# Optimization experiments

Hardware: AMD Instinct MI355X
Metric: run time of the kernel (lower is better)

Reference implementation:

```python
import jax, jax.numpy as jnp
import numpy as np

N = 14        # nodes per graph (fixed by hidden*14 in the Linear)
H = 4         # attention heads
F_IN = 128    # num_feature
C = 64        # hidden (per-head out_channels; concat=False -> mean over heads)
NEG_SLOPE = 0.2  # PyG GATConv default negative_slope


def gat_conv(x, src, dst, W, a_src, a_dst, b):
    """One PyG-style GATConv on a single graph.
    x: [N, F]  W: [F, H*C]  a_src/a_dst: [H, C]  b: [C]
    src/dst: [E] int (self-loops already appended). concat=False -> mean over heads.
    """
    h = (x @ W).reshape(N, H, C)                       # [N,H,C]
    al_src = jnp.einsum('nhc,hc->nh', h, a_src)        # [N,H]
    al_dst = jnp.einsum('nhc,hc->nh', h, a_dst)        # [N,H]
    e = jax.nn.leaky_relu(al_src[src] + al_dst[dst], NEG_SLOPE)  # [E,H]
    # softmax over incoming edges of each destination node (stable)
    m = jax.ops.segment_max(e, dst, num_segments=N)    # [N,H]
    ex = jnp.exp(e - m[dst])
    denom = jax.ops.segment_sum(ex, dst, num_segments=N)
    alpha = ex / denom[dst]                            # [E,H]
    out = jax.ops.segment_sum(alpha[:, :, None] * h[src], dst, num_segments=N)  # [N,H,C]
    return out.mean(axis=1) + b                        # [N,C]


def setup_inputs() -> dict:
    key = jax.random.key(0)
    ks = jax.random.split(key, 12)
    B, E = 16384, 182
    feature = jax.random.normal(ks[0], (B, N, F_IN), dtype=jnp.float32)
    edge_list = jax.random.randint(ks[1], (B, E, 2), 0, N, dtype=jnp.int64)

    def glorot(k, shape):
        fan = shape[0] + shape[-1]
        return jax.random.normal(k, shape, dtype=jnp.float32) * jnp.sqrt(2.0 / fan)

    return {
        'feature': feature,
        'edge_list': edge_list,
        'W1': glorot(ks[2], (F_IN, H * C)),
        'a_src1': glorot(ks[3], (H, C)),
        'a_dst1': glorot(ks[4], (H, C)),
        'b1': jnp.zeros((C,), jnp.float32),
        'W2': glorot(ks[5], (C, H * C)),
        'a_src2': glorot(ks[6], (H, C)),
        'a_dst2': glorot(ks[7], (H, C)),
        'b2': jnp.zeros((C,), jnp.float32),
        'W_lin': glorot(ks[8], (N * C, C // 2)),
        'b_lin': jnp.zeros((C // 2,), jnp.float32),
        'W_pred': glorot(ks[9], (C // 2, 1)),
        'b_pred': jnp.zeros((1,), jnp.float32),
    }


def reference(feature, edge_list, W1, a_src1, a_dst1, b1, W2, a_src2, a_dst2, b2,
              W_lin, b_lin, W_pred, b_pred):
    B = feature.shape[0]
    # PyG GATConv adds self-loops by default
    loops = jnp.broadcast_to(jnp.arange(N, dtype=edge_list.dtype), (B, N))
    src = jnp.concatenate([edge_list[..., 0], loops], axis=1)  # [B, E+N]
    dst = jnp.concatenate([edge_list[..., 1], loops], axis=1)

    def per_graph(x, s, d):
        h = jax.nn.relu(gat_conv(x, s, d, W1, a_src1, a_dst1, b1))
        # dropout is identity in eval mode
        h = gat_conv(h, s, d, W2, a_src2, a_dst2, b2)       # [N,C]
        z = h.reshape(-1) @ W_lin + b_lin                    # [C//2]
        p = z @ W_pred + b_pred                              # [1]
        return jax.nn.sigmoid(p)

    return jax.vmap(per_graph)(feature, src, dst)            # [B,1]
```

## Files before the change

kernel.cpp:

```cpp
#include <hip/hip_runtime.h>

#define NN 14
#define EE 182

typedef __attribute__((ext_vector_type(8))) short bf16x8;
typedef __attribute__((ext_vector_type(4))) short bf16x4;
typedef __attribute__((ext_vector_type(4))) float f32x4;
typedef __attribute__((ext_vector_type(4))) unsigned u32x4;
typedef __attribute__((ext_vector_type(2))) unsigned u32x2;

__device__ __forceinline__ unsigned f2bf(float f) {
    unsigned u = __float_as_uint(f);
    return (u + 0x7fffu + ((u >> 16) & 1u)) >> 16;
}
__device__ __forceinline__ unsigned pack2bf(float lo, float hi) {
    return __builtin_amdgcn_perm(__float_as_uint(hi) + 0x8000u,
                                 __float_as_uint(lo) + 0x8000u, 0x07060302u);
}
__device__ __forceinline__ bf16x8 mk8(unsigned a, unsigned b, unsigned c, unsigned d) {
    u32x4 u = {a, b, c, d};
    return __builtin_bit_cast(bf16x8, u);
}
__device__ __forceinline__ bf16x4 mk4(unsigned a, unsigned b) {
    u32x2 u = {a, b};
    return __builtin_bit_cast(bf16x4, u);
}

__global__ void prep_pack(const float* __restrict__ W1, const float* __restrict__ W2,
                          const float* __restrict__ Wl, const float* __restrict__ Wpred,
                          const float* __restrict__ bl, const float* __restrict__ bp,
                          const float* __restrict__ as1, const float* __restrict__ ad1,
                          const float* __restrict__ as2, const float* __restrict__ ad2,
                          short* __restrict__ wp1, short* __restrict__ wp2,
                          short* __restrict__ battn1, short* __restrict__ battn2,
                          float* __restrict__ wcombP) {
    int gid = blockIdx.x * 256 + threadIdx.x;
    if (gid < 32768) {
        int j = gid & 7, L = (gid >> 3) & 63, kk = (gid >> 9) & 3, nt = gid >> 11;
        int k = kk * 32 + (L >> 4) * 8 + j, n = nt * 16 + (L & 15);
        wp1[gid] = (short)f2bf(W1[k * 256 + n]);
    } else if (gid < 49152) {
        int g2 = gid - 32768;
        int j = g2 & 7, L = (g2 >> 3) & 63, kk = (g2 >> 9) & 1, nt = g2 >> 10;
        int k = kk * 32 + (L >> 4) * 8 + j, n = nt * 16 + (L & 15);
        wp2[g2] = (short)f2bf(W2[k * 256 + n]);
    } else if (gid < 51200) {
        int g2 = gid - 49152;
        int j = g2 & 7, L = (g2 >> 3) & 63, kk = g2 >> 9;
        int n = L & 15, k = kk * 32 + (L >> 4) * 8 + j;
        float val = 0.f;
        if (n < 8) {
            const float* av = ((n >> 2) ? ad1 : as1) + (n & 3) * 64;
            const float* wr = W1 + k * 256 + (n & 3) * 64;
            for (int c = 0; c < 64; ++c) val += wr[c] * av[c];
        }
        battn1[g2] = (short)f2bf(val);
    } else if (gid < 52224) {
        int g2 = gid - 51200;
        int j = g2 & 7, L = (g2 >> 3) & 63, kk = g2 >> 9;
        int n = L & 15, k = kk * 32 + (L >> 4) * 8 + j;
        float val = 0.f;
        if (n < 8) {
            const float* av = ((n >> 2) ? ad2 : as2) + (n & 3) * 64;
            const float* wr = W2 + k * 256 + (n & 3) * 64;
            for (int c = 0; c < 64; ++c) val += wr[c] * av[c];
        }
        battn2[g2] = (short)f2bf(val);
    } else if (gid < 56320) {
        int o = gid - 52224;
        int r = o & 3, i4 = o >> 2;
        int m = i4 & 15, ctq = i4 >> 4;
        int q = ctq & 3, ct = ctq >> 2;
        int chan = ct * 16 + q * 4 + r;
        float acc = 0.f;
        if (m < NN) {
            const float* wr = Wl + (m * 64 + chan) * 32;
            #pragma unroll
            for (int j = 0; j < 32; ++j) acc += wr[j] * Wpred[j];
        }
        wcombP[o] = acc;
    } else if (gid == 56320) {
        float acc = bp[0];
        #pragma unroll
        for (int j = 0; j < 32; ++j) acc += bl[j] * Wpred[j];
        wcombP[4096] = acc;
    }
}

template<int KK, bool RELU>
__device__ __forceinline__ void gat_layer2(int lane,
    const bf16x8 (*a)[KK], const short* wpB,
    const float* __restrict__ bias, const float* slabw,
    f32x4 (*o)[4], unsigned (*po)[4][2])
{
    const int m = lane & 15, q = lane >> 4;
    f32x4 agg[2][4];
    #pragma unroll
    for (int u = 0; u < 2; ++u)
        #pragma unroll
        for (int ct = 0; ct < 4; ++ct) agg[u][ct] = f32x4{0.f, 0.f, 0.f, 0.f};

    #pragma unroll
    for (int h = 0; h < 4; ++h) {
        bf16x4 P[2];
        #pragma unroll
        for (int u = 0; u < 2; ++u) {
            const float* cntf = slabw + u * 448;
            const float* alsd = cntf + 320;
            f32x4 alv = *(const f32x4*)(alsd + h * 16 + q * 4);
            float ad  = alsd[64 + h * 16 + m];
            f32x4 cv  = *(const f32x4*)(cntf + m * 20 + q * 4);
            float l0 = alv[0] + ad, l1 = alv[1] + ad, l2 = alv[2] + ad, l3 = alv[3] + ad;
            l0 = fmaxf(l0, 0.f) + 0.2f * fminf(l0, 0.f);
            l1 = fmaxf(l1, 0.f) + 0.2f * fminf(l1, 0.f);
            l2 = fmaxf(l2, 0.f) + 0.2f * fminf(l2, 0.f);
            l3 = fmaxf(l3, 0.f) + 0.2f * fminf(l3, 0.f);
            float v0 = __expf(l0) * cv[0], v1 = __expf(l1) * cv[1];
            float v2 = __expf(l2) * cv[2], v3 = __expf(l3) * cv[3];
            float s = v0 + v1 + v2 + v3;
            s += __shfl_xor(s, 16);
            s += __shfl_xor(s, 32);
            float inv = (s > 0.f) ? 0.25f / s : 0.f;
            P[u] = mk4(pack2bf(v0 * inv, v1 * inv), pack2bf(v2 * inv, v3 * inv));
        }

        #pragma unroll
        for (int ct = 0; ct < 4; ++ct) {
            f32x4 c0 = f32x4{0.f, 0.f, 0.f, 0.f}, c1 = f32x4{0.f, 0.f, 0.f, 0.f};
            #pragma unroll
            for (int kk = 0; kk < KK; ++kk) {
                bf16x8 b = *(const bf16x8*)(wpB +
                    (((h * 4 + ct) * KK + kk) * 64 + lane) * 8);
                c0 = __builtin_amdgcn_mfma_f32_16x16x32_bf16(a[0][kk], b, c0, 0, 0, 0);
                c1 = __builtin_amdgcn_mfma_f32_16x16x32_bf16(a[1][kk], b, c1, 0, 0, 0);
            }
            agg[0][ct] = __builtin_amdgcn_mfma_f32_16x16x16bf16_1k(
                mk4(pack2bf(c0[0], c0[1]), pack2bf(c0[2], c0[3])), P[0], agg[0][ct], 0, 0, 0);
            agg[1][ct] = __builtin_amdgcn_mfma_f32_16x16x16bf16_1k(
                mk4(pack2bf(c1[0], c1[1]), pack2bf(c1[2], c1[3])), P[1], agg[1][ct], 0, 0, 0);
        }
    }

    #pragma unroll
    for (int ct = 0; ct < 4; ++ct) {
        float4 bb = *(const float4*)(bias + ct * 16 + q * 4);
        #pragma unroll
        for (int u = 0; u < 2; ++u) {
            float o0 = agg[u][ct][0] + bb.x, o1 = agg[u][ct][1] + bb.y;
            float o2v = agg[u][ct][2] + bb.z, o3 = agg[u][ct][3] + bb.w;
            if (RELU) {
                o0 = fmaxf(o0, 0.f);  o1 = fmaxf(o1, 0.f);
                o2v = fmaxf(o2v, 0.f); o3 = fmaxf(o3, 0.f);
                if (m >= NN) { o0 = 0.f; o1 = 0.f; o2v = 0.f; o3 = 0.f; }
                po[u][ct][0] = pack2bf(o0, o1);
                po[u][ct][1] = pack2bf(o2v, o3);
            } else {
                o[u][ct] = f32x4{o0, o1, o2v, o3};
            }
        }
    }
}

__global__ __launch_bounds__(1024, 4) void gat_fused(
    const float* __restrict__ feature,
    const int*   __restrict__ edge_list,
    const float* __restrict__ b1, const float* __restrict__ b2,
    const short* __restrict__ wpck,
    const float* __restrict__ wcombP,
    float* __restrict__ out, int B)
{
    const int w = threadIdx.x >> 6, lane = threadIdx.x & 63;
    const int m = lane & 15, q = lane >> 4;

    __shared__ __align__(16) short    swts[52224];
    __shared__ __align__(16) unsigned slab[16 * 896];

    float* slabw = (float*)(slab + w * 896);

    {
        const u32x4* srcw = (const u32x4*)wpck;
        u32x4* dstw = (u32x4*)swts;
        #pragma unroll
        for (int r = 0; r < 7; ++r) {
            int i = r * 1024 + (int)threadIdx.x;
            if (i < 6528) dstw[i] = srcw[i];
        }
    }
    __syncthreads();

    const short* swp1  = swts;
    const short* swp2  = swts + 32768;
    const short* sbat1 = swts + 49152;
    const short* sbat2 = swts + 51200;

    const int g0 = blockIdx.x * 64 + w * 4;

    #pragma clang loop unroll(disable)
    for (int it = 0; it < 2; ++it) {
        const int g = g0 + it * 2;
        if (g >= B) break;
        const bool act1 = (g + 1) < B;
        float* cnt0 = slabw;
        float* cnt1 = slabw + 448;

        #pragma unroll
        for (int i = 0; i < 5; ++i) {
            cnt0[i * 64 + lane] = 0.f;
            cnt1[i * 64 + lane] = 0.f;
        }
        {
            const int2* ep0 = (const int2*)edge_list + (size_t)g * EE;
            const int2* ep1 = ep0 + EE;
            #pragma unroll
            for (int r = 0; r < 3; ++r) {
                int i = r * 64 + lane;
                if (i < EE) {
                    int2 e0 = ep0[i];
                    atomicAdd(&cnt0[e0.y * 20 + e0.x], 1.f);
                    if (act1) { int2 e1 = ep1[i]; atomicAdd(&cnt1[e1.y * 20 + e1.x], 1.f); }
                }
            }
            if (lane < NN) {
                atomicAdd(&cnt0[lane * 21], 1.f);
                if (act1) atomicAdd(&cnt1[lane * 21], 1.f);
            }
        }

        bf16x8 a1[2][4];
        #pragma unroll
        for (int u = 0; u < 2; ++u)
            #pragma unroll
            for (int kk = 0; kk < 4; ++kk) a1[u][kk] = mk8(0, 0, 0, 0);
        if (m < NN) {
            const float* xg0 = feature + (size_t)g * (NN * 128) + m * 128;
            #pragma unroll
            for (int kk = 0; kk < 4; ++kk) {
                float4 v0 = *(const float4*)(xg0 + kk * 32 + q * 8);
                float4 v1 = *(const float4*)(xg0 + kk * 32 + q * 8 + 4);
                a1[0][kk] = mk8(pack2bf(v0.x, v0.y), pack2bf(v0.z, v0.w),
                                pack2bf(v1.x, v1.y), pack2bf(v1.z, v1.w));
            }
        }
        if (act1 && m < NN) {
            const float* xg1 = feature + (size_t)(g + 1) * (NN * 128) + m * 128;
            #pragma unroll
            for (int kk = 0; kk < 4; ++kk) {
                float4 v0 = *(const float4*)(xg1 + kk * 32 + q * 8);
                float4 v1 = *(const float4*)(xg1 + kk * 32 + q * 8 + 4);
                a1[1][kk] = mk8(pack2bf(v0.x, v0.y), pack2bf(v0.z, v0.w),
                                pack2bf(v1.x, v1.y), pack2bf(v1.z, v1.w));
            }
        }

        {
            f32x4 ca0 = f32x4{0.f, 0.f, 0.f, 0.f}, ca1 = f32x4{0.f, 0.f, 0.f, 0.f};
            #pragma unroll
            for (int kk = 0; kk < 4; ++kk) {
                bf16x8 b = *(const bf16x8*)(sbat1 + (kk * 64 + lane) * 8);
                ca0 = __builtin_amdgcn_mfma_f32_16x16x32_bf16(a1[0][kk], b, ca0, 0, 0, 0);
                ca1 = __builtin_amdgcn_mfma_f32_16x16x32_bf16(a1[1][kk], b, ca1, 0, 0, 0);
            }
            if (m < 8) {
                int off = (m >> 2) * 64 + (m & 3) * 16 + q * 4;
                *(f32x4*)(slabw + 320 + off) = ca0;
                *(f32x4*)(slabw + 448 + 320 + off) = ca1;
            }
        }

        unsigned po1[2][4][2];
        gat_layer2<4, true>(lane, a1, swp1, b1, slabw, nullptr, po1);

        bf16x8 a2[2][2];
        {
            int ad0 = ((q & 1) * 32 + m) * 4;
            int ad1_ = ad0 + 64;
            bool hi = (q >> 1) != 0;
            #pragma unroll
            for (int u = 0; u < 2; ++u)
            #pragma unroll
            for (int kk = 0; kk < 2; ++kk) {
                unsigned sA0 = __builtin_amdgcn_ds_bpermute(ad0, (int)po1[u][2 * kk][0]);
                unsigned sA1 = __builtin_amdgcn_ds_bpermute(ad0, (int)po1[u][2 * kk][1]);
                unsigned sB0 = __builtin_amdgcn_ds_bpermute(ad0, (int)po1[u][2 * kk + 1][0]);
                unsigned sB1 = __builtin_amdgcn_ds_bpermute(ad0, (int)po1[u][2 * kk + 1][1]);
                unsigned tA0 = __builtin_amdgcn_ds_bpermute(ad1_, (int)po1[u][2 * kk][0]);
                unsigned tA1 = __builtin_amdgcn_ds_bpermute(ad1_, (int)po1[u][2 * kk][1]);
                unsigned tB0 = __builtin_amdgcn_ds_bpermute(ad1_, (int)po1[u][2 * kk + 1][0]);
                unsigned tB1 = __builtin_amdgcn_ds_bpermute(ad1_, (int)po1[u][2 * kk + 1][1]);
                a2[u][kk] = mk8(hi ? sB0 : sA0, hi ? sB1 : sA1,
                                hi ? tB0 : tA0, hi ? tB1 : tA1);
            }
        }

        {
            f32x4 ca0 = f32x4{0.f, 0.f, 0.f, 0.f}, ca1 = f32x4{0.f, 0.f, 0.f, 0.f};
            #pragma unroll
            for (int kk = 0; kk < 2; ++kk) {
                bf16x8 b = *(const bf16x8*)(sbat2 + (kk * 64 + lane) * 8);
                ca0 = __builtin_amdgcn_mfma_f32_16x16x32_bf16(a2[0][kk], b, ca0, 0, 0, 0);
                ca1 = __builtin_amdgcn_mfma_f32_16x16x32_bf16(a2[1][kk], b, ca1, 0, 0, 0);
            }
            if (m < 8) {
                int off = (m >> 2) * 64 + (m & 3) * 16 + q * 4;
                *(f32x4*)(slabw + 320 + off) = ca0;
                *(f32x4*)(slabw + 448 + 320 + off) = ca1;
            }
        }

        f32x4 o2[2][4];
        gat_layer2<2, false>(lane, a2, swp2, b2, slabw, o2, nullptr);

        float p0 = 0.f, p1 = 0.f;
        #pragma unroll
        for (int ct = 0; ct < 4; ++ct) {
            float4 wv = *(const float4*)(wcombP + ((ct * 4 + q) * 16 + m) * 4);
            p0 += o2[0][ct][0] * wv.x + o2[0][ct][1] * wv.y +
                  o2[0][ct][2] * wv.z + o2[0][ct][3] * wv.w;
            p1 += o2[1][ct][0] * wv.x + o2[1][ct][1] * wv.y +
                  o2[1][ct][2] * wv.z + o2[1][ct][3] * wv.w;
        }
        p0 += __shfl_xor(p0, 1);  p1 += __shfl_xor(p1, 1);
        p0 += __shfl_xor(p0, 2);  p1 += __shfl_xor(p1, 2);
        p0 += __shfl_xor(p0, 4);  p1 += __shfl_xor(p1, 4);
        p0 += __shfl_xor(p0, 8);  p1 += __shfl_xor(p1, 8);
        p0 += __shfl_xor(p0, 16); p1 += __shfl_xor(p1, 16);
        p0 += __shfl_xor(p0, 32); p1 += __shfl_xor(p1, 32);
        if (lane == 0) {
            float cc = wcombP[4096];
            out[g] = 1.f / (1.f + __expf(-(p0 + cc)));
            if (act1) out[g + 1] = 1.f / (1.f + __expf(-(p1 + cc)));
        }
    }
}

extern "C" void kernel_launch(void* const* d_in, const int* in_sizes, int n_in,
                              void* d_out, int out_size, void* d_ws, size_t ws_size,
                              hipStream_t stream) {
    const float* feature = (const float*)d_in[0];
    const int*   edges   = (const int*)d_in[1];
    const float* W1  = (const float*)d_in[2];
    const float* as1 = (const float*)d_in[3];
    const float* ad1 = (const float*)d_in[4];
    const float* b1  = (const float*)d_in[5];
    const float* W2  = (const float*)d_in[6];
    const float* as2 = (const float*)d_in[7];
    const float* ad2 = (const float*)d_in[8];
    const float* b2  = (const float*)d_in[9];
    const float* Wl  = (const float*)d_in[10];
    const float* bl  = (const float*)d_in[11];
    const float* Wp  = (const float*)d_in[12];
    const float* bp  = (const float*)d_in[13];
    float* out = (float*)d_out;

    short* wp1    = (short*)d_ws;
    short* wp2    = wp1 + 32768;
    short* battn1 = wp2 + 16384;
    short* battn2 = battn1 + 2048;
    float* wcombP = (float*)(battn2 + 1024);

    prep_pack<<<221, 256, 0, stream>>>(W1, W2, Wl, Wp, bl, bp, as1, ad1, as2, ad2,
                                       wp1, wp2, battn1, battn2, wcombP);

    const int B = in_sizes[0] / (NN * 128);
    gat_fused<<<(B + 63) / 64, 1024, 0, stream>>>(feature, edges, b1, b2,
                                                  wp1, wcombP, out, B);
}
```

Baseline: 234.1 us.

## Prefetch next graph pair during layer 1 and pack edge counts into bytes

Unrolls the two-iteration per-wave loop into two process_pair calls. The first call issues the feature loads and edge scatter for the second pair after its layer-1 work, so global-memory latency overlaps with MFMA compute. Edge multiplicity counts move from float LDS atomics to byte-packed uint atomics, which shrinks the per-wave LDS slab and lets each gat_layer2 read its counts with one dword load. The softmax coefficients for all heads are also computed before the MFMA loop. In exchange, register pressure rises (two sets of a1 fragments live at once, plus P[4][2]), and byte counts would overflow if more than 255 edges repeat on one pair, which cannot happen with 182 edges.

```diff
diff --git a/kernel.cpp b/kernel.cpp
--- a/kernel.cpp
+++ b/kernel.cpp
@@ -87,43 +87,84 @@
     }
 }
 
+__device__ __forceinline__ void scatter_edges(int lane, const int2* ep,
+                                              unsigned char* cnt, bool act) {
+    if (!act) return;
+    #pragma unroll
+    for (int r = 0; r < 3; ++r) {
+        int i = r * 64 + lane;
+        if (i < EE) {
+            int2 e = ep[i];
+            int b = e.y * 20 + e.x;
+            atomicAdd((unsigned*)(cnt + (b & ~3)), 1u << ((b & 3) * 8));
+        }
+    }
+    if (lane < NN) {
+        int b = lane * 21;
+        atomicAdd((unsigned*)(cnt + (b & ~3)), 1u << ((b & 3) * 8));
+    }
+}
+
+__device__ __forceinline__ void load_a1(const float* __restrict__ feature,
+                                        int g, int m, int q, bool act, bf16x8* dst) {
+    if (act && m < NN) {
+        const float* xg = feature + (size_t)g * (NN * 128) + m * 128;
+        #pragma unroll
+        for (int kk = 0; kk < 4; ++kk) {
+            float4 v0 = *(const float4*)(xg + kk * 32 + q * 8);
+            float4 v1 = *(const float4*)(xg + kk * 32 + q * 8 + 4);
+            dst[kk] = mk8(pack2bf(v0.x, v0.y), pack2bf(v0.z, v0.w),
+                          pack2bf(v1.x, v1.y), pack2bf(v1.z, v1.w));
+        }
+    } else {
+        #pragma unroll
+        for (int kk = 0; kk < 4; ++kk) dst[kk] = mk8(0, 0, 0, 0);
+    }
+}
+
 template<int KK, bool RELU>
 __device__ __forceinline__ void gat_layer2(int lane,
     const bf16x8 (*a)[KK], const short* wpB,
-    const float* __restrict__ bias, const float* slabw,
+    const float* __restrict__ bias,
+    const unsigned char* cntb, const float* alsd,
     f32x4 (*o)[4], unsigned (*po)[4][2])
 {
     const int m = lane & 15, q = lane >> 4;
-    f32x4 agg[2][4];
-    #pragma unroll
-    for (int u = 0; u < 2; ++u)
-        #pragma unroll
-        for (int ct = 0; ct < 4; ++ct) agg[u][ct] = f32x4{0.f, 0.f, 0.f, 0.f};
-
+
+    bf16x4 P[4][2];
     #pragma unroll
     for (int h = 0; h < 4; ++h) {
-        bf16x4 P[2];
         #pragma unroll
         for (int u = 0; u < 2; ++u) {
-            const float* cntf = slabw + u * 448;
-            const float* alsd = cntf + 320;
-            f32x4 alv = *(const f32x4*)(alsd + h * 16 + q * 4);
-            float ad  = alsd[64 + h * 16 + m];
-            f32x4 cv  = *(const f32x4*)(cntf + m * 20 + q * 4);
+            const float* alsdu = alsd + u * 128;
+            f32x4 alv = *(const f32x4*)(alsdu + h * 16 + q * 4);
+            float ad  = alsdu[64 + h * 16 + m];
+            unsigned cw = *(const unsigned*)(cntb + u * 320 + m * 20 + q * 4);
             float l0 = alv[0] + ad, l1 = alv[1] + ad, l2 = alv[2] + ad, l3 = alv[3] + ad;
             l0 = fmaxf(l0, 0.f) + 0.2f * fminf(l0, 0.f);
             l1 = fmaxf(l1, 0.f) + 0.2f * fminf(l1, 0.f);
             l2 = fmaxf(l2, 0.f) + 0.2f * fminf(l2, 0.f);
             l3 = fmaxf(l3, 0.f) + 0.2f * fminf(l3, 0.f);
-            float v0 = __expf(l0) * cv[0], v1 = __expf(l1) * cv[1];
-            float v2 = __expf(l2) * cv[2], v3 = __expf(l3) * cv[3];
+            float v0 = __expf(l0) * (float)(cw & 255u);
+            float v1 = __expf(l1) * (float)((cw >> 8) & 255u);
+            float v2 = __expf(l2) * (float)((cw >> 16) & 255u);
+            float v3 = __expf(l3) * (float)(cw >> 24);
             float s = v0 + v1 + v2 + v3;
             s += __shfl_xor(s, 16);
             s += __shfl_xor(s, 32);
             float inv = (s > 0.f) ? 0.25f / s : 0.f;
-            P[u] = mk4(pack2bf(v0 * inv, v1 * inv), pack2bf(v2 * inv, v3 * inv));
-        }
-
+            P[h][u] = mk4(pack2bf(v0 * inv, v1 * inv), pack2bf(v2 * inv, v3 * inv));
+        }
+    }
+
+    f32x4 agg[2][4];
+    #pragma unroll
+    for (int u = 0; u < 2; ++u)
+        #pragma unroll
+        for (int ct = 0; ct < 4; ++ct) agg[u][ct] = f32x4{0.f, 0.f, 0.f, 0.f};
+
+    #pragma unroll
+    for (int h = 0; h < 4; ++h) {
         #pragma unroll
         for (int ct = 0; ct < 4; ++ct) {
             f32x4 c0 = f32x4{0.f, 0.f, 0.f, 0.f}, c1 = f32x4{0.f, 0.f, 0.f, 0.f};
@@ -135,9 +176,9 @@
                 c1 = __builtin_amdgcn_mfma_f32_16x16x32_bf16(a[1][kk], b, c1, 0, 0, 0);
             }
             agg[0][ct] = __builtin_amdgcn_mfma_f32_16x16x16bf16_1k(
-                mk4(pack2bf(c0[0], c0[1]), pack2bf(c0[2], c0[3])), P[0], agg[0][ct], 0, 0, 0);
+                mk4(pack2bf(c0[0], c0[1]), pack2bf(c0[2], c0[3])), P[h][0], agg[0][ct], 0, 0, 0);
             agg[1][ct] = __builtin_amdgcn_mfma_f32_16x16x16bf16_1k(
-                mk4(pack2bf(c1[0], c1[1]), pack2bf(c1[2], c1[3])), P[1], agg[1][ct], 0, 0, 0);
+                mk4(pack2bf(c1[0], c1[1]), pack2bf(c1[2], c1[3])), P[h][1], agg[1][ct], 0, 0, 0);
         }
     }
 
@@ -161,6 +202,108 @@
     }
 }
 
+template<bool PRE>
+__device__ __forceinline__ void process_pair(
+    int lane, int g, bool act1,
+    const bf16x8 (*a1)[4],
+    unsigned char* cntb, float* alsd,
+    const short* swp1, const short* swp2, const short* sbat1, const short* sbat2,
+    const float* __restrict__ b1, const float* __restrict__ b2,
+    const float* __restrict__ wcombP, float* __restrict__ out, int B,
+    const float* __restrict__ feature, const int* __restrict__ edge_list,
+    int gN, unsigned char* cntbN, bf16x8 (*a1N)[4])
+{
+    const int m = lane & 15, q = lane >> 4;
+
+    {
+        f32x4 ca0 = f32x4{0.f, 0.f, 0.f, 0.f}, ca1 = f32x4{0.f, 0.f, 0.f, 0.f};
+        #pragma unroll
+        for (int kk = 0; kk < 4; ++kk) {
+            bf16x8 b = *(const bf16x8*)(sbat1 + (kk * 64 + lane) * 8);
+            ca0 = __builtin_amdgcn_mfma_f32_16x16x32_bf16(a1[0][kk], b, ca0, 0, 0, 0);
+            ca1 = __builtin_amdgcn_mfma_f32_16x16x32_bf16(a1[1][kk], b, ca1, 0, 0, 0);
+        }
+        if (m < 8) {
+            int off = (m >> 2) * 64 + (m & 3) * 16 + q * 4;
+            *(f32x4*)(alsd + off) = ca0;
+            *(f32x4*)(alsd + 128 + off) = ca1;
+        }
+    }
+
+    unsigned po1[2][4][2];
+    gat_layer2<4, true>(lane, a1, swp1, b1, cntb, alsd, nullptr, po1);
+
+    if (PRE) {
+        bool aN0 = gN < B, aN1 = gN + 1 < B;
+        load_a1(feature, gN, m, q, aN0, a1N[0]);
+        load_a1(feature, gN + 1, m, q, aN1, a1N[1]);
+        const int2* ep = (const int2*)edge_list + (size_t)gN * EE;
+        scatter_edges(lane, ep, cntbN, aN0);
+        scatter_edges(lane, ep + EE, cntbN + 320, aN1);
+    }
+
+    bf16x8 a2[2][2];
+    {
+        int ad0 = ((q & 1) * 32 + m) * 4;
+        int ad1_ = ad0 + 64;
+        bool hi = (q >> 1) != 0;
+        #pragma unroll
+        for (int u = 0; u < 2; ++u)
+        #pragma unroll
+        for (int kk = 0; kk < 2; ++kk) {
+            unsigned sA0 = __builtin_amdgcn_ds_bpermute(ad0, (int)po1[u][2 * kk][0]);
+            unsigned sA1 = __builtin_amdgcn_ds_bpermute(ad0, (int)po1[u][2 * kk][1]);
+            unsigned sB0 = __builtin_amdgcn_ds_bpermute(ad0, (int)po1[u][2 * kk + 1][0]);
+            unsigned sB1 = __builtin_amdgcn_ds_bpermute(ad0, (int)po1[u][2 * kk + 1][1]);
+            unsigned tA0 = __builtin_amdgcn_ds_bpermute(ad1_, (int)po1[u][2 * kk][0]);
+            unsigned tA1 = __builtin_amdgcn_ds_bpermute(ad1_, (int)po1[u][2 * kk][1]);
+            unsigned tB0 = __builtin_amdgcn_ds_bpermute(ad1_, (int)po1[u][2 * kk + 1][0]);
+            unsigned tB1 = __builtin_amdgcn_ds_bpermute(ad1_, (int)po1[u][2 * kk + 1][1]);
+            a2[u][kk] = mk8(hi ? sB0 : sA0, hi ? sB1 : sA1,
+                            hi ? tB0 : tA0, hi ? tB1 : tA1);
+        }
+    }
+
+    {
+        f32x4 ca0 = f32x4{0.f, 0.f, 0.f, 0.f}, ca1 = f32x4{0.f, 0.f, 0.f, 0.f};
+        #pragma unroll
+        for (int kk = 0; kk < 2; ++kk) {
+            bf16x8 b = *(const bf16x8*)(sbat2 + (kk * 64 + lane) * 8);
+            ca0 = __builtin_amdgcn_mfma_f32_16x16x32_bf16(a2[0][kk], b, ca0, 0, 0, 0);
+            ca1 = __builtin_amdgcn_mfma_f32_16x16x32_bf16(a2[1][kk], b, ca1, 0, 0, 0);
+        }
+        if (m < 8) {
+            int off = (m >> 2) * 64 + (m & 3) * 16 + q * 4;
+            *(f32x4*)(alsd + off) = ca0;
+            *(f32x4*)(alsd + 128 + off) = ca1;
+        }
+    }
+
+    f32x4 o2[2][4];
+    gat_layer2<2, false>(lane, a2, swp2, b2, cntb, alsd, o2, nullptr);
+
+    float p0 = 0.f, p1 = 0.f;
+    #pragma unroll
+    for (int ct = 0; ct < 4; ++ct) {
+        float4 wv = *(const float4*)(wcombP + ((ct * 4 + q) * 16 + m) * 4);
+        p0 += o2[0][ct][0] * wv.x + o2[0][ct][1] * wv.y +
+              o2[0][ct][2] * wv.z + o2[0][ct][3] * wv.w;
+        p1 += o2[1][ct][0] * wv.x + o2[1][ct][1] * wv.y +
+              o2[1][ct][2] * wv.z + o2[1][ct][3] * wv.w;
+    }
+    p0 += __shfl_xor(p0, 1);  p1 += __shfl_xor(p1, 1);
+    p0 += __shfl_xor(p0, 2);  p1 += __shfl_xor(p1, 2);
+    p0 += __shfl_xor(p0, 4);  p1 += __shfl_xor(p1, 4);
+    p0 += __shfl_xor(p0, 8);  p1 += __shfl_xor(p1, 8);
+    p0 += __shfl_xor(p0, 16); p1 += __shfl_xor(p1, 16);
+    p0 += __shfl_xor(p0, 32); p1 += __shfl_xor(p1, 32);
+    if (lane == 0) {
+        float cc = wcombP[4096];
+        out[g] = 1.f / (1.f + __expf(-(p0 + cc)));
+        if (act1) out[g + 1] = 1.f / (1.f + __expf(-(p1 + cc)));
+    }
+}
+
 __global__ __launch_bounds__(1024, 4) void gat_fused(
     const float* __restrict__ feature,
     const int*   __restrict__ edge_list,
@@ -173,9 +316,11 @@
     const int m = lane & 15, q = lane >> 4;
 
     __shared__ __align__(16) short    swts[52224];
-    __shared__ __align__(16) unsigned slab[16 * 896];
-
-    float* slabw = (float*)(slab + w * 896);
+    __shared__ __align__(16) unsigned slab[16 * 576];
+
+    unsigned* swave = slab + w * 576;
+    unsigned char* cntb = (unsigned char*)swave;
+    float* alsd = (float*)(swave + 320);
 
     {
         const u32x4* srcw = (const u32x4*)wpck;
@@ -194,143 +339,28 @@
     const short* sbat2 = swts + 51200;
 
     const int g0 = blockIdx.x * 64 + w * 4;
-
-    #pragma clang loop unroll(disable)
-    for (int it = 0; it < 2; ++it) {
-        const int g = g0 + it * 2;
-        if (g >= B) break;
-        const bool act1 = (g + 1) < B;
-        float* cnt0 = slabw;
-        float* cnt1 = slabw + 448;
-
-        #pragma unroll
-        for (int i = 0; i < 5; ++i) {
-            cnt0[i * 64 + lane] = 0.f;
-            cnt1[i * 64 + lane] = 0.f;
-        }
-        {
-            const int2* ep0 = (const int2*)edge_list + (size_t)g * EE;
-            const int2* ep1 = ep0 + EE;
-            #pragma unroll
-            for (int r = 0; r < 3; ++r) {
-                int i = r * 64 + lane;
-                if (i < EE) {
-                    int2 e0 = ep0[i];
-                    atomicAdd(&cnt0[e0.y * 20 + e0.x], 1.f);
-                    if (act1) { int2 e1 = ep1[i]; atomicAdd(&cnt1[e1.y * 20 + e1.x], 1.f); }
-                }
-            }
-            if (lane < NN) {
-                atomicAdd(&cnt0[lane * 21], 1.f);
-                if (act1) atomicAdd(&cnt1[lane * 21], 1.f);
-            }
-        }
-
-        bf16x8 a1[2][4];
-        #pragma unroll
-        for (int u = 0; u < 2; ++u)
-            #pragma unroll
-            for (int kk = 0; kk < 4; ++kk) a1[u][kk] = mk8(0, 0, 0, 0);
-        if (m < NN) {
-            const float* xg0 = feature + (size_t)g * (NN * 128) + m * 128;
-            #pragma unroll
-            for (int kk = 0; kk < 4; ++kk) {
-                float4 v0 = *(const float4*)(xg0 + kk * 32 + q * 8);
-                float4 v1 = *(const float4*)(xg0 + kk * 32 + q * 8 + 4);
-                a1[0][kk] = mk8(pack2bf(v0.x, v0.y), pack2bf(v0.z, v0.w),
-                                pack2bf(v1.x, v1.y), pack2bf(v1.z, v1.w));
-            }
-        }
-        if (act1 && m < NN) {
-            const float* xg1 = feature + (size_t)(g + 1) * (NN * 128) + m * 128;
-            #pragma unroll
-            for (int kk = 0; kk < 4; ++kk) {
-                float4 v0 = *(const float4*)(xg1 + kk * 32 + q * 8);
-                float4 v1 = *(const float4*)(xg1 + kk * 32 + q * 8 + 4);
-                a1[1][kk] = mk8(pack2bf(v0.x, v0.y), pack2bf(v0.z, v0.w),
-                                pack2bf(v1.x, v1.y), pack2bf(v1.z, v1.w));
-            }
-        }
-
-        {
-            f32x4 ca0 = f32x4{0.f, 0.f, 0.f, 0.f}, ca1 = f32x4{0.f, 0.f, 0.f, 0.f};
-            #pragma unroll
-            for (int kk = 0; kk < 4; ++kk) {
-                bf16x8 b = *(const bf16x8*)(sbat1 + (kk * 64 + lane) * 8);
-                ca0 = __builtin_amdgcn_mfma_f32_16x16x32_bf16(a1[0][kk], b, ca0, 0, 0, 0);
-                ca1 = __builtin_amdgcn_mfma_f32_16x16x32_bf16(a1[1][kk], b, ca1, 0, 0, 0);
-            }
-            if (m < 8) {
-                int off = (m >> 2) * 64 + (m & 3) * 16 + q * 4;
-                *(f32x4*)(slabw + 320 + off) = ca0;
-                *(f32x4*)(slabw + 448 + 320 + off) = ca1;
-            }
-        }
-
-        unsigned po1[2][4][2];
-        gat_layer2<4, true>(lane, a1, swp1, b1, slabw, nullptr, po1);
-
-        bf16x8 a2[2][2];
-        {
-            int ad0 = ((q & 1) * 32 + m) * 4;
-            int ad1_ = ad0 + 64;
-            bool hi = (q >> 1) != 0;
-            #pragma unroll
-            for (int u = 0; u < 2; ++u)
-            #pragma unroll
-            for (int kk = 0; kk < 2; ++kk) {
-                unsigned sA0 = __builtin_amdgcn_ds_bpermute(ad0, (int)po1[u][2 * kk][0]);
-                unsigned sA1 = __builtin_amdgcn_ds_bpermute(ad0, (int)po1[u][2 * kk][1]);
-                unsigned sB0 = __builtin_amdgcn_ds_bpermute(ad0, (int)po1[u][2 * kk + 1][0]);
-                unsigned sB1 = __builtin_amdgcn_ds_bpermute(ad0, (int)po1[u][2 * kk + 1][1]);
-                unsigned tA0 = __builtin_amdgcn_ds_bpermute(ad1_, (int)po1[u][2 * kk][0]);
-                unsigned tA1 = __builtin_amdgcn_ds_bpermute(ad1_, (int)po1[u][2 * kk][1]);
-                unsigned tB0 = __builtin_amdgcn_ds_bpermute(ad1_, (int)po1[u][2 * kk + 1][0]);
-                unsigned tB1 = __builtin_amdgcn_ds_bpermute(ad1_, (int)po1[u][2 * kk + 1][1]);
-                a2[u][kk] = mk8(hi ? sB0 : sA0, hi ? sB1 : sA1,
-                                hi ? tB0 : tA0, hi ? tB1 : tA1);
-            }
-        }
-
-        {
-            f32x4 ca0 = f32x4{0.f, 0.f, 0.f, 0.f}, ca1 = f32x4{0.f, 0.f, 0.f, 0.f};
-            #pragma unroll
-            for (int kk = 0; kk < 2; ++kk) {
-                bf16x8 b = *(const bf16x8*)(sbat2 + (kk * 64 + lane) * 8);
-                ca0 = __builtin_amdgcn_mfma_f32_16x16x32_bf16(a2[0][kk], b, ca0, 0, 0, 0);
-                ca1 = __builtin_amdgcn_mfma_f32_16x16x32_bf16(a2[1][kk], b, ca1, 0, 0, 0);
-            }
-            if (m < 8) {
-                int off = (m >> 2) * 64 + (m & 3) * 16 + q * 4;
-                *(f32x4*)(slabw + 320 + off) = ca0;
-                *(f32x4*)(slabw + 448 + 320 + off) = ca1;
-            }
-        }
-
-        f32x4 o2[2][4];
-        gat_layer2<2, false>(lane, a2, swp2, b2, slabw, o2, nullptr);
-
-        float p0 = 0.f, p1 = 0.f;
-        #pragma unroll
-        for (int ct = 0; ct < 4; ++ct) {
-            float4 wv = *(const float4*)(wcombP + ((ct * 4 + q) * 16 + m) * 4);
-            p0 += o2[0][ct][0] * wv.x + o2[0][ct][1] * wv.y +
-                  o2[0][ct][2] * wv.z + o2[0][ct][3] * wv.w;
-            p1 += o2[1][ct][0] * wv.x + o2[1][ct][1] * wv.y +
-                  o2[1][ct][2] * wv.z + o2[1][ct][3] * wv.w;
-        }
-        p0 += __shfl_xor(p0, 1);  p1 += __shfl_xor(p1, 1);
-        p0 += __shfl_xor(p0, 2);  p1 += __shfl_xor(p1, 2);
-        p0 += __shfl_xor(p0, 4);  p1 += __shfl_xor(p1, 4);
-        p0 += __shfl_xor(p0, 8);  p1 += __shfl_xor(p1, 8);
-        p0 += __shfl_xor(p0, 16); p1 += __shfl_xor(p1, 16);
-        p0 += __shfl_xor(p0, 32); p1 += __shfl_xor(p1, 32);
-        if (lane == 0) {
-            float cc = wcombP[4096];
-            out[g] = 1.f / (1.f + __expf(-(p0 + cc)));
-            if (act1) out[g + 1] = 1.f / (1.f + __expf(-(p1 + cc)));
-        }
-    }
+    const bool aA1 = g0 + 1 < B, aB0 = g0 + 2 < B, aB1 = g0 + 3 < B;
+
+    #pragma unroll
+    for (int i = 0; i < 5; ++i) swave[i * 64 + lane] = 0u;
+
+    {
+        const int2* ep = (const int2*)edge_list + (size_t)g0 * EE;
+        scatter_edges(lane, ep, cntb, true);
+        scatter_edges(lane, ep + EE, cntb + 320, aA1);
+    }
+    bf16x8 a1A[2][4];
+    load_a1(feature, g0, m, q, true, a1A[0]);
+    load_a1(feature, g0 + 1, m, q, aA1, a1A[1]);
+
+    bf16x8 a1B[2][4];
+    process_pair<true>(lane, g0, aA1, a1A, cntb, alsd,
+                       swp1, swp2, sbat1, sbat2, b1, b2, wcombP, out, B,
+                       feature, edge_list, g0 + 2, cntb + 640, a1B);
+    if (aB0)
+        process_pair<false>(lane, g0 + 2, aB1, a1B, cntb + 640, alsd,
+                            swp1, swp2, sbat1, sbat2, b1, b2, wcombP, out, B,
+                            feature, edge_list, 0, cntb, a1B);
 }
 
 extern "C" void kernel_launch(void* const* d_in, const int* in_sizes, int n_in,
```

Measured after the change: 458.1 us. 1.96x slower.
